# Kernel optimization log

Hardware: AMD Instinct MI355X
Metric: run time of the kernel (lower is better)

Reference implementation:

```python
import jax, jax.numpy as jnp
import numpy as np

B, S, D, H = 4, 2048, 512, 8
E = D // H  # d_head = 64

def setup_inputs() -> dict:
    key = jax.random.key(0)
    ks = jax.random.split(key, 10)
    s_in = (1.0 / np.sqrt(D))
    x  = jax.random.normal(ks[0], (B, S, D), dtype=jnp.float32)
    Wq = jax.random.normal(ks[1], (H, D, E), dtype=jnp.float32) * s_in
    bq = jax.random.normal(ks[2], (H, E), dtype=jnp.float32) * 0.01
    Wk = jax.random.normal(ks[3], (H, D, E), dtype=jnp.float32) * s_in
    bk = jax.random.normal(ks[4], (H, E), dtype=jnp.float32) * 0.01
    Wv = jax.random.normal(ks[5], (H, D, E), dtype=jnp.float32) * s_in
    bv = jax.random.normal(ks[6], (H, E), dtype=jnp.float32) * 0.01
    Wo = jax.random.normal(ks[7], (D, D), dtype=jnp.float32) * s_in
    bo = jax.random.normal(ks[8], (D,), dtype=jnp.float32) * 0.01
    return {"x": x, "Wq": Wq, "bq": bq, "Wk": Wk, "bk": bk,
            "Wv": Wv, "bv": bv, "Wo": Wo, "bo": bo}

def reference(x, Wq, bq, Wk, bk, Wv, bv, Wo, bo):
    B_, S_, D_ = x.shape
    # per-head projections (batched over head axis h)
    q = jnp.einsum('bsd,hde->bhse', x, Wq) + bq[None, :, None, :]
    k = jnp.einsum('bsd,hde->bhse', x, Wk) + bk[None, :, None, :]
    v = jnp.einsum('bsd,hde->bhse', x, Wv) + bv[None, :, None, :]
    # NOTE: original scales by d_model**-0.5 (full D), not d_head**-0.5
    scale = jnp.asarray(D_, x.dtype) ** -0.5
    scores = jnp.einsum('bhse,bhte->bhst', q, k) * scale  # [B,H,S,S]
    causal = jnp.tril(jnp.ones((S_, S_), dtype=bool))
    scores = jnp.where(causal[None, None], scores, -jnp.inf)
    attn = jax.nn.softmax(scores, axis=-1)
    out = jnp.einsum('bhst,bhte->bhse', attn, v)  # [B,H,S,E]
    # concat heads along feature dim (head-major), matching torch.cat
    out = out.transpose(0, 2, 1, 3).reshape(B_, S_, D_)
    return out @ Wo + bo  # final projection; dropout never applied in source
```

## Files before the change

kernel.cpp:

```cpp
#include <hip/hip_runtime.h>

typedef unsigned short u16;
typedef __bf16 bf16x8 __attribute__((ext_vector_type(8)));
typedef short s16x4 __attribute__((ext_vector_type(4)));
typedef short s16x8 __attribute__((ext_vector_type(8)));
typedef float f32x4 __attribute__((ext_vector_type(4)));

#define BB 4
#define SS 2048
#define DD 512
#define HH 8
#define EE 64
#define MM 8192
#define BHSE (BB*HH*SS*EE)

#define GLOBAL_AS __attribute__((address_space(1)))
#define LDS_AS    __attribute__((address_space(3)))

__device__ __forceinline__ float b2f(u16 u) {
    return __uint_as_float(((unsigned int)u) << 16);
}
__device__ __forceinline__ u16 f2b(float f) {
    unsigned int v = __float_as_uint(f);
    v += 0x7fffu + ((v >> 16) & 1u);
    return (u16)(v >> 16);
}
__device__ __forceinline__ float loadE(const void* p, size_t idx, int isbf16) {
    return isbf16 ? b2f(((const u16*)p)[idx]) : ((const float*)p)[idx];
}
__device__ __forceinline__ void load_lds16(const u16* g, u16* l) {
    __builtin_amdgcn_global_load_lds((GLOBAL_AS void*)g, (LDS_AS void*)l, 16, 0, 0);
}

__device__ __forceinline__ int detect_bf16_wave(const u16* x) {
    const int lane = threadIdx.x & 63;
    float a0 = fabsf(b2f(x[2 * lane]));
    float a1 = fabsf(b2f(x[2 * (lane + 64)]));
    int c0 = (a0 == 0.f) || (a0 > 1e-4f && a0 < 100.f);
    int c1 = (a1 == 0.f) || (a1 > 1e-4f && a1 < 100.f);
    int cnt = __popcll(__ballot(c0)) + __popcll(__ballot(c1));
    return cnt >= 96;
}

__global__ __launch_bounds__(256) void prep(
    const void* __restrict__ X,
    const void* __restrict__ Wq, const void* __restrict__ Wk,
    const void* __restrict__ Wv, const void* __restrict__ Wo,
    u16* __restrict__ Xb, u16* __restrict__ WT, u16* __restrict__ WoT,
    int* __restrict__ flag)
{
    const int isbf16 = detect_bf16_wave((const u16*)X);
    const int bid = blockIdx.x;
    const int tid = threadIdx.x;
    if (bid < 1024) {
        if (bid == 0 && tid == 0) *flag = isbf16;
        const size_t i0 = ((size_t)bid * 256 + tid) * 16;
        if (isbf16) {
            const uint4* src = (const uint4*)(((const u16*)X) + i0);
            uint4* dst = (uint4*)(Xb + i0);
            dst[0] = src[0];
            dst[1] = src[1];
        } else {
            const float* xf = ((const float*)X) + i0;
            float4 f0 = *(const float4*)xf;
            float4 f1 = *(const float4*)(xf + 4);
            float4 f2 = *(const float4*)(xf + 8);
            float4 f3 = *(const float4*)(xf + 12);
            u16 tmp[16] = { f2b(f0.x), f2b(f0.y), f2b(f0.z), f2b(f0.w),
                            f2b(f1.x), f2b(f1.y), f2b(f1.z), f2b(f1.w),
                            f2b(f2.x), f2b(f2.y), f2b(f2.z), f2b(f2.w),
                            f2b(f3.x), f2b(f3.y), f2b(f3.z), f2b(f3.w) };
            *(uint4*)(Xb + i0) = *(const uint4*)tmp;
            *(uint4*)(Xb + i0 + 8) = *(const uint4*)(tmp + 8);
        }
        return;
    }
    const int j = bid - 1024;
    const int job = j >> 6;
    const int t = j & 63;
    const void* src; u16* dst; int src_ld;
    if (job < 3) {
        const void* W = (job == 0) ? Wq : ((job == 1) ? Wk : Wv);
        int h = t >> 3, kt = t & 7;
        size_t off = (size_t)h * DD * EE + (size_t)kt * 64 * EE;
        src = isbf16 ? (const void*)(((const u16*)W) + off)
                     : (const void*)(((const float*)W) + off);
        src_ld = EE;
        dst = WT + (size_t)job * 512 * 512 + (size_t)(h * 64) * 512 + kt * 64;
    } else {
        int a = t >> 3, b = t & 7;
        size_t off = (size_t)(a * 64) * 512 + b * 64;
        src = isbf16 ? (const void*)(((const u16*)Wo) + off)
                     : (const void*)(((const float*)Wo) + off);
        src_ld = 512;
        dst = WoT + (size_t)(b * 64) * 512 + a * 64;
    }
    __shared__ __align__(16) u16 Ts[64 * 72];
#pragma unroll
    for (int it = 0; it < 2; ++it) {
        int idx = it * 256 + tid;
        int r = idx >> 3, c = (idx & 7) << 3;
        u16 tmp[8];
        if (isbf16) {
            *(bf16x8*)tmp = *(const bf16x8*)(((const u16*)src) + (size_t)r * src_ld + c);
        } else {
            const float* sp = ((const float*)src) + (size_t)r * src_ld + c;
            float4 f0 = *(const float4*)sp;
            float4 f1 = *(const float4*)(sp + 4);
            tmp[0] = f2b(f0.x); tmp[1] = f2b(f0.y); tmp[2] = f2b(f0.z); tmp[3] = f2b(f0.w);
            tmp[4] = f2b(f1.x); tmp[5] = f2b(f1.y); tmp[6] = f2b(f1.z); tmp[7] = f2b(f1.w);
        }
#pragma unroll
        for (int k = 0; k < 8; ++k) Ts[(c + k) * 72 + r] = tmp[k];
    }
    __syncthreads();
#pragma unroll
    for (int it = 0; it < 2; ++it) {
        int idx = it * 256 + tid;
        int r = idx >> 3, c = (idx & 7) << 3;
        *(bf16x8*)(dst + (size_t)r * 512 + c) = *(const bf16x8*)&Ts[r * 72 + c];
    }
}

template<int MT, int NT>
__device__ __forceinline__ void mfma_step(const u16* As, const u16* Bs,
    int mh, int nh, int lq, int quad, f32x4 acc[MT][NT])
{
    const int sw = lq & 7;
#pragma unroll
    for (int kw = 0; kw < 2; ++kw) {
        const int G = kw * 4 + quad;
        const int col = ((G ^ sw) << 3);
        bf16x8 a[MT], b[NT];
#pragma unroll
        for (int mt = 0; mt < MT; ++mt)
            a[mt] = *(const bf16x8*)&As[(mh + mt * 16 + lq) * 64 + col];
#pragma unroll
        for (int nt = 0; nt < NT; ++nt)
            b[nt] = *(const bf16x8*)&Bs[(nh + nt * 16 + lq) * 64 + col];
#pragma unroll
        for (int mt = 0; mt < MT; ++mt)
#pragma unroll
            for (int nt = 0; nt < NT; ++nt)
                acc[mt][nt] = __builtin_amdgcn_mfma_f32_16x16x32_bf16(a[mt], b[nt], acc[mt][nt], 0, 0, 0);
    }
}

__global__ __launch_bounds__(256) void gemm_qkv(
    const u16* __restrict__ Xb, const u16* __restrict__ WT,
    const void* __restrict__ bq, const void* __restrict__ bk,
    const void* __restrict__ bv, u16* __restrict__ qkv,
    const int* __restrict__ flag)
{
    const float SCALE = 0.04419417382415922f;
    const int isbf16 = *flag;
    const int l = blockIdx.x;
    const int m0 = ((l & 7) * 8 + ((l >> 3) & 7)) * 128;
    const int n0 = (l >> 6) * 128;
    const int tid = threadIdx.x;
    const int wave = tid >> 6, lane = tid & 63;
    const int lq = lane & 15, quad = lane >> 4;
    const int mh = (wave & 1) * 64, nh = (wave >> 1) * 64;
    __shared__ __align__(16) u16 As[128 * 64];
    __shared__ __align__(16) u16 Bs[128 * 64];
    f32x4 acc[4][4] = {};

    const int swz = (lane & 7) ^ ((lane >> 3) & 7);
    const size_t lane_off = (size_t)(lane >> 3) * 512 + 8 * swz;

    for (int k0 = 0; k0 < 512; k0 += 64) {
        __syncthreads();
#pragma unroll
        for (int jj = 0; jj < 4; ++jj) {
            const int c = wave * 4 + jj;
            load_lds16(Xb + (size_t)(m0 + 8 * c) * 512 + k0 + lane_off, &As[c * 512]);
            load_lds16(WT + (size_t)(n0 + 8 * c) * 512 + k0 + lane_off, &Bs[c * 512]);
        }
        __syncthreads();
        mfma_step<4, 4>(As, Bs, mh, nh, lq, quad, acc);
    }

    const int proj = n0 >> 9;
    const void* bias = (proj == 0) ? bq : ((proj == 1) ? bk : bv);
#pragma unroll
    for (int mt = 0; mt < 4; ++mt) {
#pragma unroll
        for (int nt = 0; nt < 4; ++nt) {
#pragma unroll
            for (int r = 0; r < 4; ++r) {
                int m = m0 + mh + mt * 16 + quad * 4 + r;
                int n = n0 + nh + nt * 16 + lq;
                int nn = n & 511;
                float v = acc[mt][nt][r] + loadE(bias, nn, isbf16);
                if (proj == 0) v *= SCALE;
                int b_ = m >> 11, s = m & 2047, h = nn >> 6, e = nn & 63;
                qkv[(size_t)proj * BHSE + (((size_t)(b_ * HH + h) * SS + s) * EE + e)] = f2b(v);
            }
        }
    }
}

struct VStage { uint4 va, vb; };

__device__ __forceinline__ void stageK_dma(const u16* Kh, int t0, u16* Ksb, int tid) {
    const int wave = tid >> 6, lane = tid & 63;
    const int r = lane >> 3, s = lane & 7;
#pragma unroll
    for (int jj = 0; jj < 2; ++jj) {
        const int c = wave * 2 + jj;
        const u16* g = Kh + (size_t)(t0 + 8 * c + r) * 64 + ((s ^ (r & 7)) << 3);
        load_lds16(g, Ksb + c * 512);
    }
}
__device__ __forceinline__ void stageV_load(VStage& st, const u16* Vh, int t0, int tid) {
    int t2 = 2 * (tid & 31), e8 = (tid >> 5) * 8;
    st.va = *(const uint4*)(Vh + (size_t)(t0 + t2) * 64 + e8);
    st.vb = *(const uint4*)(Vh + (size_t)(t0 + t2 + 1) * 64 + e8);
}
__device__ __forceinline__ void stageV_write(const VStage& st, u16* VTsb, int tid) {
    int t2 = 2 * (tid & 31), e8 = (tid >> 5) * 8;
    int g2 = ((t2 >> 2) & 3) * 16 + ((t2 >> 4) << 2) + (t2 & 3);
    const unsigned* pa = (const unsigned*)&st.va;
    const unsigned* pb = (const unsigned*)&st.vb;
#pragma unroll
    for (int k = 0; k < 4; ++k) {
        unsigned lo = __builtin_amdgcn_perm(pb[k], pa[k], 0x05040100u);
        unsigned hi = __builtin_amdgcn_perm(pb[k], pa[k], 0x07060302u);
        *(unsigned*)(VTsb + (e8 + 2 * k) * 72 + g2) = lo;
        *(unsigned*)(VTsb + (e8 + 2 * k + 1) * 72 + g2) = hi;
    }
}

__device__ __forceinline__ void attn_tile2(const u16* Ksb, const u16* VTsb,
    const bf16x8* qf0, const bf16x8* qf1, int lq, int quad, int qh, int th,
    bool diag, f32x4 Ot[4][2], f32x4* lfrag)
{
    const int p0 = (quad ^ (lq & 7)) << 3;
    f32x4 sc[2][2];
#pragma unroll
    for (int tj = 0; tj < 2; ++tj) {
        const u16* Krow = Ksb + ((th * 2 + tj) * 16 + lq) * 64;
        bf16x8 k0 = *(const bf16x8*)(Krow + p0);
        bf16x8 k1 = *(const bf16x8*)(Krow + (p0 ^ 32));
        __builtin_amdgcn_s_setprio(1);
#pragma unroll
        for (int f = 0; f < 2; ++f) {
            f32x4 s = {};
            s = __builtin_amdgcn_mfma_f32_16x16x32_bf16(k0, qf0[f], s, 0, 0, 0);
            s = __builtin_amdgcn_mfma_f32_16x16x32_bf16(k1, qf1[f], s, 0, 0, 0);
            sc[f][tj] = s;
        }
        __builtin_amdgcn_s_setprio(0);
    }
    union { unsigned u[4]; bf16x8 v; } ones;
    ones.u[0] = ones.u[1] = ones.u[2] = ones.u[3] = 0x3F803F80u;
    bf16x8 pf[2];
#pragma unroll
    for (int f = 0; f < 2; ++f) {
        unsigned pu[8];
#pragma unroll
        for (int tj = 0; tj < 2; ++tj)
#pragma unroll
            for (int r = 0; r < 4; ++r) {
                float p = __expf(sc[f][tj][r]);
                if (diag) {
                    int tl = (th * 2 + tj) * 16 + quad * 4 + r;
                    int ql = qh * 32 + f * 16 + lq;
                    p = (tl <= ql) ? p : 0.f;
                }
                pu[tj * 4 + r] = __float_as_uint(p);
            }
        union { unsigned u[4]; bf16x8 v; } w;
        w.u[0] = __builtin_amdgcn_perm(pu[1], pu[0], 0x07060302u);
        w.u[1] = __builtin_amdgcn_perm(pu[3], pu[2], 0x07060302u);
        w.u[2] = __builtin_amdgcn_perm(pu[5], pu[4], 0x07060302u);
        w.u[3] = __builtin_amdgcn_perm(pu[7], pu[6], 0x07060302u);
        pf[f] = w.v;
        lfrag[f] = __builtin_amdgcn_mfma_f32_16x16x32_bf16(ones.v, w.v, lfrag[f], 0, 0, 0);
    }
    __builtin_amdgcn_s_setprio(1);
#pragma unroll
    for (int et = 0; et < 4; ++et) {
        bf16x8 vf = *(const bf16x8*)(VTsb + (et * 16 + lq) * 72 + quad * 16 + th * 8);
#pragma unroll
        for (int f = 0; f < 2; ++f)
            Ot[et][f] = __builtin_amdgcn_mfma_f32_16x16x32_bf16(vf, pf[f], Ot[et][f], 0, 0, 0);
    }
    __builtin_amdgcn_s_setprio(0);
}

#define WAITV(N) asm volatile("s_waitcnt vmcnt(" #N ")" ::: "memory")
#define SBAR0()  __builtin_amdgcn_sched_barrier(0)

#define ATTN_ITER(i, CUR, STOLD, STNEW)                                        \
  {                                                                            \
    const bool m1 = ((i) + 1 <= nIt), m2 = ((i) + 2 <= nIt);                   \
    if (m1) stageK_dma(Kh, (tFirst + (i) + 1) * 64, Ks[(CUR) ^ 1], tid);       \
    SBAR0();                                                                   \
    if (m2) stageV_load(STNEW, Vh, (tFirst + (i) + 2) * 64, tid);              \
    SBAR0();                                                                   \
    attn_tile2(Ks[CUR], VTs[CUR], qf0, qf1, lq, quad, qh, th,                  \
               diagHere && ((i) == nIt), Ot, lfrag);                           \
    if (m1) {                                                                  \
      if (m2) { WAITV(4); } else { WAITV(2); }                                 \
      stageV_write(STOLD, VTs[(CUR) ^ 1], tid);                                \
      if (m2) { WAITV(2); } else { WAITV(0); }                                 \
    }                                                                          \
    asm volatile("s_waitcnt lgkmcnt(0)" ::: "memory");                         \
    __builtin_amdgcn_s_barrier();                                              \
    SBAR0();                                                                   \
  }

__global__ __launch_bounds__(256, 4) void attn_kernel(
    const u16* __restrict__ Qg, const u16* __restrict__ Kg,
    const u16* __restrict__ Vg, u16* __restrict__ Og,
    float* __restrict__ Opart, float* __restrict__ Lpart)
{
    const int bh = blockIdx.x;
    const int j  = (int)gridDim.y - 1 - (int)blockIdx.y;
    const int c  = blockIdx.z;
    if (c && j < 16) return;
    const int qb = j * 64;
    const int tFirst = c * 16;
    const int tLast  = (j < tFirst + 15) ? j : (tFirst + 15);
    const int nIt = tLast - tFirst;
    const bool diagHere = (tLast == j);
    const bool partial = (j >= 16);

    const int tid = threadIdx.x;
    const int wave = tid >> 6, lane = tid & 63;
    const int lq = lane & 15, quad = lane >> 4;
    const int qh = wave & 1, th = wave >> 1;
    const int b = bh >> 3, h = bh & 7;

    const size_t base = (size_t)bh * SS * EE;
    const u16* Kh = Kg + base;
    const u16* Vh = Vg + base;

    __shared__ __align__(16) u16 Ks[2][64 * 64];
    __shared__ __align__(16) u16 VTs[2][64 * 72];

    bf16x8 qf0[2], qf1[2];
#pragma unroll
    for (int f = 0; f < 2; ++f) {
        const int qrow_f = qb + qh * 32 + f * 16 + lq;
        const u16* Qp = Qg + base + (size_t)qrow_f * EE;
        qf0[f] = *(const bf16x8*)(Qp + quad * 8);
        qf1[f] = *(const bf16x8*)(Qp + 32 + quad * 8);
    }

    f32x4 Ot[4][2] = {};
    f32x4 lfrag[2] = {};
    VStage stA, stB;

    stageK_dma(Kh, tFirst * 64, Ks[0], tid);
    SBAR0();
    stageV_load(stA, Vh, tFirst * 64, tid);
    SBAR0();
    if (nIt >= 1) {
        stageV_load(stB, Vh, (tFirst + 1) * 64, tid);
        SBAR0();
        WAITV(2);
    } else {
        WAITV(0);
    }
    stageV_write(stA, VTs[0], tid);
    asm volatile("s_waitcnt lgkmcnt(0)" ::: "memory");
    __builtin_amdgcn_s_barrier();
    SBAR0();

    for (int i = 0; ; i += 2) {
        ATTN_ITER(i, 0, stB, stA);
        if (i + 1 > nIt) break;
        ATTN_ITER(i + 1, 1, stA, stB);
        if (i + 2 > nIt) break;
    }

    __syncthreads();
    float* redO = (float*)&Ks[0][0];
    float* redL = (float*)&VTs[0][0];
    if (th == 1) {
#pragma unroll
        for (int et = 0; et < 4; ++et)
#pragma unroll
            for (int f = 0; f < 2; ++f)
                *(f32x4*)&redO[(((qh * 4 + et) * 2 + f) * 64 + lane) * 4] = Ot[et][f];
#pragma unroll
        for (int f = 0; f < 2; ++f)
            redL[(qh * 2 + f) * 64 + lane] = lfrag[f][0];
    }
    __syncthreads();
    if (th == 1) return;
    float lf[2];
#pragma unroll
    for (int f = 0; f < 2; ++f)
        lf[f] = lfrag[f][0] + redL[(qh * 2 + f) * 64 + lane];
#pragma unroll
    for (int et = 0; et < 4; ++et)
#pragma unroll
        for (int f = 0; f < 2; ++f)
            Ot[et][f] += *(const f32x4*)&redO[(((qh * 4 + et) * 2 + f) * 64 + lane) * 4];

    if (!partial) {
#pragma unroll
        for (int f = 0; f < 2; ++f) {
            const float inv = 1.f / lf[f];
            const int qrow_f = qb + qh * 32 + f * 16 + lq;
            u16* Op = Og + (((size_t)(b * SS + qrow_f)) * HH + h) * EE;
#pragma unroll
            for (int et = 0; et < 4; ++et) {
                u16 tmp[4];
#pragma unroll
                for (int r = 0; r < 4; ++r) tmp[r] = f2b(Ot[et][f][r] * inv);
                *(uint2*)(Op + et * 16 + quad * 4) = *(const uint2*)tmp;
            }
        }
    } else {
        const size_t slot = ((size_t)(bh * 16 + (j - 16)) * 2 + c);
        float* Os = Opart + slot * 4096;
#pragma unroll
        for (int f = 0; f < 2; ++f) {
            const int ql = qh * 32 + f * 16 + lq;
#pragma unroll
            for (int et = 0; et < 4; ++et)
                *(f32x4*)&Os[ql * 64 + et * 16 + quad * 4] = Ot[et][f];
            if (quad == 0) Lpart[slot * 64 + ql] = lf[f];
        }
    }
}

__global__ __launch_bounds__(256) void attn_merge(
    const float* __restrict__ Opart, const float* __restrict__ Lpart,
    u16* __restrict__ Og)
{
    const int tg = blockIdx.x * 256 + threadIdx.x;
    const int e8 = (tg & 7) * 8;
    const int rest = tg >> 3;
    const int bh = rest >> 10;
    const int sp = rest & 1023;
    const int jj = sp >> 6;
    const int ql = sp & 63;
    const size_t slot = (size_t)(bh * 16 + jj) * 2;
    const size_t o0 = slot * 4096 + (size_t)ql * 64 + e8;
    float4 a0 = *(const float4*)&Opart[o0];
    float4 a1 = *(const float4*)&Opart[o0 + 4];
    float4 b0 = *(const float4*)&Opart[o0 + 4096];
    float4 b1 = *(const float4*)&Opart[o0 + 4096 + 4];
    const size_t ls = slot * 64 + ql;
    const float inv = 1.f / (Lpart[ls] + Lpart[ls + 64]);
    const int b = bh >> 3, h = bh & 7;
    const int s = 1024 + sp;
    u16 tmp[8];
    tmp[0] = f2b((a0.x + b0.x) * inv);
    tmp[1] = f2b((a0.y + b0.y) * inv);
    tmp[2] = f2b((a0.z + b0.z) * inv);
    tmp[3] = f2b((a0.w + b0.w) * inv);
    tmp[4] = f2b((a1.x + b1.x) * inv);
    tmp[5] = f2b((a1.y + b1.y) * inv);
    tmp[6] = f2b((a1.z + b1.z) * inv);
    tmp[7] = f2b((a1.w + b1.w) * inv);
    u16* Op = Og + (((size_t)(b * SS + s)) * HH + h) * EE + e8;
    *(uint4*)Op = *(const uint4*)tmp;
}

__global__ __launch_bounds__(256) void gemm_out(
    const u16* __restrict__ A, const u16* __restrict__ WoT,
    const void* __restrict__ bo, void* __restrict__ out,
    const int* __restrict__ flag)
{
    const int isbf16 = *flag;
    const int l = blockIdx.x;
    const int m0 = ((l & 7) * 8 + ((l >> 3) & 7)) * 128;
    const int n0 = (l >> 6) * 64;
    const int tid = threadIdx.x;
    const int wave = tid >> 6, lane = tid & 63;
    const int lq = lane & 15, quad = lane >> 4;
    const int mh = (wave & 1) * 64, nh = (wave >> 1) * 32;
    __shared__ __align__(16) u16 As[128 * 64];
    __shared__ __align__(16) u16 Bs[64 * 64];
    f32x4 acc[4][2] = {};

    const int swz = (lane & 7) ^ ((lane >> 3) & 7);
    const size_t lane_off = (size_t)(lane >> 3) * 512 + 8 * swz;

    for (int k0 = 0; k0 < 512; k0 += 64) {
        __syncthreads();
#pragma unroll
        for (int jj = 0; jj < 4; ++jj) {
            const int c = wave * 4 + jj;
            load_lds16(A + (size_t)(m0 + 8 * c) * 512 + k0 + lane_off, &As[c * 512]);
        }
#pragma unroll
        for (int jj = 0; jj < 2; ++jj) {
            const int c = wave * 2 + jj;
            load_lds16(WoT + (size_t)(n0 + 8 * c) * 512 + k0 + lane_off, &Bs[c * 512]);
        }
        __syncthreads();
        mfma_step<4, 2>(As, Bs, mh, nh, lq, quad, acc);
    }
#pragma unroll
    for (int mt = 0; mt < 4; ++mt) {
#pragma unroll
        for (int nt = 0; nt < 2; ++nt) {
#pragma unroll
            for (int r = 0; r < 4; ++r) {
                int m = m0 + mh + mt * 16 + quad * 4 + r;
                int n = n0 + nh + nt * 16 + lq;
                float v = acc[mt][nt][r] + loadE(bo, n, isbf16);
                if (isbf16) ((u16*)out)[(size_t)m * 512 + n] = f2b(v);
                else        ((float*)out)[(size_t)m * 512 + n] = v;
            }
        }
    }
}

extern "C" void kernel_launch(void* const* d_in, const int* in_sizes, int n_in,
                              void* d_out, int out_size, void* d_ws, size_t ws_size,
                              hipStream_t stream) {
    const void* x  = d_in[0];
    const void* Wq = d_in[1];
    const void* bq = d_in[2];
    const void* Wk = d_in[3];
    const void* bk = d_in[4];
    const void* Wv = d_in[5];
    const void* bv = d_in[6];
    const void* Wo = d_in[7];
    const void* bo = d_in[8];

    u16* WT   = (u16*)d_ws;
    u16* WoT  = WT + 3 * 512 * 512;
    u16* qkv  = WoT + 512 * 512;
    u16* attn = qkv + 3 * (size_t)BHSE;
    int* flag = (int*)(attn + (size_t)BHSE);
    u16* Xb   = (u16*)(flag + 8);
    float* Opart = (float*)(Xb + (size_t)MM * DD);
    float* Lpart = Opart + (size_t)1024 * 4096;

    prep<<<1024 + 256, 256, 0, stream>>>(x, Wq, Wk, Wv, Wo, Xb, WT, WoT, flag);
    gemm_qkv<<<(MM / 128) * (1536 / 128), 256, 0, stream>>>(Xb, WT, bq, bk, bv, qkv, flag);
    attn_kernel<<<dim3(BB * HH, SS / 64, 2), 256, 0, stream>>>(
        qkv, qkv + BHSE, qkv + 2 * (size_t)BHSE, attn, Opart, Lpart);
    attn_merge<<<1024, 256, 0, stream>>>(Opart, Lpart, attn);
    gemm_out<<<(MM / 128) * (512 / 64), 256, 0, stream>>>(attn, WoT, bo, d_out, flag);
}
```

Baseline: 176.3 us.

## Double-buffer LDS tiles in QKV and output projection GEMMs

Both projection GEMMs now use two LDS buffers per operand. The load for k-tile k+2 is issued right after the MFMA step on tile k, with explicit vmcnt waits and barriers replacing the load-sync-compute loop. The aim is to hide global-to-LDS latency behind the MFMA work. The cost is doubled shared memory per block (64KB for the QKV GEMM), which may reduce occupancy.

```diff
diff --git a/kernel.cpp b/kernel.cpp
--- a/kernel.cpp
+++ b/kernel.cpp
@@ -16,6 +16,10 @@
 
 #define GLOBAL_AS __attribute__((address_space(1)))
 #define LDS_AS    __attribute__((address_space(3)))
+
+#define WAITV(N)    asm volatile("s_waitcnt vmcnt(" #N ")" ::: "memory")
+#define WAITLGKM0() asm volatile("s_waitcnt lgkmcnt(0)" ::: "memory")
+#define SBAR0()     __builtin_amdgcn_sched_barrier(0)
 
 __device__ __forceinline__ float b2f(u16 u) {
     return __uint_as_float(((unsigned int)u) << 16);
@@ -161,24 +165,42 @@
     const int wave = tid >> 6, lane = tid & 63;
     const int lq = lane & 15, quad = lane >> 4;
     const int mh = (wave & 1) * 64, nh = (wave >> 1) * 64;
-    __shared__ __align__(16) u16 As[128 * 64];
-    __shared__ __align__(16) u16 Bs[128 * 64];
+    __shared__ __align__(16) u16 As[2][128 * 64];
+    __shared__ __align__(16) u16 Bs[2][128 * 64];
     f32x4 acc[4][4] = {};
 
     const int swz = (lane & 7) ^ ((lane >> 3) & 7);
     const size_t lane_off = (size_t)(lane >> 3) * 512 + 8 * swz;
 
-    for (int k0 = 0; k0 < 512; k0 += 64) {
-        __syncthreads();
-#pragma unroll
-        for (int jj = 0; jj < 4; ++jj) {
-            const int c = wave * 4 + jj;
-            load_lds16(Xb + (size_t)(m0 + 8 * c) * 512 + k0 + lane_off, &As[c * 512]);
-            load_lds16(WT + (size_t)(n0 + 8 * c) * 512 + k0 + lane_off, &Bs[c * 512]);
-        }
-        __syncthreads();
-        mfma_step<4, 4>(As, Bs, mh, nh, lq, quad, acc);
-    }
+#define QKV_STAGE(KT, BI)                                                      \
+    {                                                                          \
+        _Pragma("unroll")                                                      \
+        for (int jj = 0; jj < 4; ++jj) {                                       \
+            const int ch = wave * 4 + jj;                                      \
+            load_lds16(Xb + (size_t)(m0 + 8 * ch) * 512 + (KT) * 64 + lane_off,\
+                       &As[BI][ch * 512]);                                     \
+            load_lds16(WT + (size_t)(n0 + 8 * ch) * 512 + (KT) * 64 + lane_off,\
+                       &Bs[BI][ch * 512]);                                     \
+        }                                                                      \
+    }
+
+    QKV_STAGE(0, 0); SBAR0();
+    QKV_STAGE(1, 1); SBAR0();
+    WAITV(8);
+    __builtin_amdgcn_s_barrier(); SBAR0();
+
+    for (int k = 0; k < 8; ++k) {
+        const int cur = k & 1;
+        mfma_step<4, 4>(&As[cur][0], &Bs[cur][0], mh, nh, lq, quad, acc);
+        if (k == 7) break;
+        WAITLGKM0(); SBAR0();
+        __builtin_amdgcn_s_barrier();
+        if (k + 2 < 8) { QKV_STAGE(k + 2, cur); SBAR0(); WAITV(8); }
+        else           { WAITV(0); }
+        __builtin_amdgcn_s_barrier();
+        SBAR0();
+    }
+#undef QKV_STAGE
 
     const int proj = n0 >> 9;
     const void* bias = (proj == 0) ? bq : ((proj == 1) ? bk : bv);
@@ -289,9 +311,6 @@
     __builtin_amdgcn_s_setprio(0);
 }
 
-#define WAITV(N) asm volatile("s_waitcnt vmcnt(" #N ")" ::: "memory")
-#define SBAR0()  __builtin_amdgcn_sched_barrier(0)
-
 #define ATTN_ITER(i, CUR, STOLD, STNEW)                                        \
   {                                                                            \
     const bool m1 = ((i) + 1 <= nIt), m2 = ((i) + 2 <= nIt);                   \
@@ -306,7 +325,7 @@
       stageV_write(STOLD, VTs[(CUR) ^ 1], tid);                                \
       if (m2) { WAITV(2); } else { WAITV(0); }                                 \
     }                                                                          \
-    asm volatile("s_waitcnt lgkmcnt(0)" ::: "memory");                         \
+    WAITLGKM0();                                                               \
     __builtin_amdgcn_s_barrier();                                              \
     SBAR0();                                                                   \
   }
@@ -365,7 +384,7 @@
         WAITV(0);
     }
     stageV_write(stA, VTs[0], tid);
-    asm volatile("s_waitcnt lgkmcnt(0)" ::: "memory");
+    WAITLGKM0();
     __builtin_amdgcn_s_barrier();
     SBAR0();
 
@@ -476,28 +495,47 @@
     const int wave = tid >> 6, lane = tid & 63;
     const int lq = lane & 15, quad = lane >> 4;
     const int mh = (wave & 1) * 64, nh = (wave >> 1) * 32;
-    __shared__ __align__(16) u16 As[128 * 64];
-    __shared__ __align__(16) u16 Bs[64 * 64];
+    __shared__ __align__(16) u16 As[2][128 * 64];
+    __shared__ __align__(16) u16 Bs[2][64 * 64];
     f32x4 acc[4][2] = {};
 
     const int swz = (lane & 7) ^ ((lane >> 3) & 7);
     const size_t lane_off = (size_t)(lane >> 3) * 512 + 8 * swz;
 
-    for (int k0 = 0; k0 < 512; k0 += 64) {
-        __syncthreads();
-#pragma unroll
-        for (int jj = 0; jj < 4; ++jj) {
-            const int c = wave * 4 + jj;
-            load_lds16(A + (size_t)(m0 + 8 * c) * 512 + k0 + lane_off, &As[c * 512]);
-        }
-#pragma unroll
-        for (int jj = 0; jj < 2; ++jj) {
-            const int c = wave * 2 + jj;
-            load_lds16(WoT + (size_t)(n0 + 8 * c) * 512 + k0 + lane_off, &Bs[c * 512]);
-        }
-        __syncthreads();
-        mfma_step<4, 2>(As, Bs, mh, nh, lq, quad, acc);
-    }
+#define OUT_STAGE(KT, BI)                                                      \
+    {                                                                          \
+        _Pragma("unroll")                                                      \
+        for (int jj = 0; jj < 4; ++jj) {                                       \
+            const int ch = wave * 4 + jj;                                      \
+            load_lds16(A + (size_t)(m0 + 8 * ch) * 512 + (KT) * 64 + lane_off, \
+                       &As[BI][ch * 512]);                                     \
+        }                                                                      \
+        _Pragma("unroll")                                                      \
+        for (int jj = 0; jj < 2; ++jj) {                                       \
+            const int ch = wave * 2 + jj;                                      \
+            load_lds16(WoT + (size_t)(n0 + 8 * ch) * 512 + (KT) * 64 + lane_off,\
+                       &Bs[BI][ch * 512]);                                     \
+        }                                                                      \
+    }
+
+    OUT_STAGE(0, 0); SBAR0();
+    OUT_STAGE(1, 1); SBAR0();
+    WAITV(6);
+    __builtin_amdgcn_s_barrier(); SBAR0();
+
+    for (int k = 0; k < 8; ++k) {
+        const int cur = k & 1;
+        mfma_step<4, 2>(&As[cur][0], &Bs[cur][0], mh, nh, lq, quad, acc);
+        if (k == 7) break;
+        WAITLGKM0(); SBAR0();
+        __builtin_amdgcn_s_barrier();
+        if (k + 2 < 8) { OUT_STAGE(k + 2, cur); SBAR0(); WAITV(6); }
+        else           { WAITV(0); }
+        __builtin_amdgcn_s_barrier();
+        SBAR0();
+    }
+#undef OUT_STAGE
+
 #pragma unroll
     for (int mt = 0; mt < 4; ++mt) {
 #pragma unroll
```

Measured after the change: 190.5 us. +8.1%, slower.
